# Kernel optimization log

Measured on AMD Instinct MI355X. Metric: run time of the kernel, lower is better.

## Reference

```python
import jax, jax.numpy as jnp
import numpy as np
from jax import lax

B, C, H, W = 16, 128, 96, 96
G, S = 4, 2            # DySample groups, scale
CO = 2 * G * S * S     # offset channels = 32
COUT = 64              # EUCB2 out_channels
BN_EPS = 1e-5


def conv2d(x, w, pad=0, dil=1, groups=1):
    return lax.conv_general_dilated(
        x, w, (1, 1), [(pad, pad), (pad, pad)],
        rhs_dilation=(dil, dil), feature_group_count=groups,
        dimension_numbers=('NCHW', 'OIHW', 'NCHW'))


def init_pos():
    # torch: arange((-s+1)/2,(s-1)/2+1)/s ; meshgrid ij ; stack ; transpose(1,2) ; repeat(1,G,1)
    h = (jnp.arange(S, dtype=jnp.float32) - (S - 1) / 2) / S
    gy, gx = jnp.meshgrid(h, h, indexing='ij')
    m = jnp.stack([gy, gx])                 # [2,S,S]
    m = jnp.swapaxes(m, 1, 2)               # transpose(1,2)
    m = jnp.tile(m, (1, G, 1))              # [2, S*G, S]
    return m.reshape(1, -1, 1, 1)           # [1, 2*G*S^2, 1, 1]


def grid_sample_border(x, grid):
    # x: [N,Cg,H,W], grid: [N,Ho,Wo,2] (x,y in [-1,1]), align_corners=False, border pad
    N, Cg, Hi, Wi = x.shape
    Ho, Wo = grid.shape[1], grid.shape[2]
    ix = jnp.clip(((grid[..., 0] + 1.0) * Wi - 1.0) * 0.5, 0.0, Wi - 1.0)
    iy = jnp.clip(((grid[..., 1] + 1.0) * Hi - 1.0) * 0.5, 0.0, Hi - 1.0)
    x0f = jnp.floor(ix); y0f = jnp.floor(iy)
    wx = (ix - x0f)[:, None]                # [N,1,Ho,Wo]
    wy = (iy - y0f)[:, None]
    x0 = jnp.clip(x0f.astype(jnp.int32), 0, Wi - 1)
    x1 = jnp.clip(x0 + 1, 0, Wi - 1)
    y0 = jnp.clip(y0f.astype(jnp.int32), 0, Hi - 1)
    y1 = jnp.clip(y0 + 1, 0, Hi - 1)
    flat = x.reshape(N, Cg, Hi * Wi)

    def gather(yi, xi):
        idx = (yi * Wi + xi).reshape(N, -1)
        return jax.vmap(lambda f, i: f[:, i])(flat, idx).reshape(N, Cg, Ho, Wo)

    v00 = gather(y0, x0); v01 = gather(y0, x1)
    v10 = gather(y1, x0); v11 = gather(y1, x1)
    return (v00 * (1 - wx) * (1 - wy) + v01 * wx * (1 - wy)
            + v10 * (1 - wx) * wy + v11 * wx * wy)


def setup_inputs() -> dict:
    key = jax.random.key(0)
    ks = jax.random.split(key, 11)
    inp = {
        'x': jax.random.normal(ks[0], (B, C, H, W), jnp.float32),
        'Wo1': jax.random.normal(ks[1], (CO, C, 1, 1), jnp.float32) * 0.001,
        'bo1': jnp.zeros((CO,), jnp.float32),
        'Wo2': jax.random.normal(ks[2], (CO, CO, 3, 3), jnp.float32) * 0.001,
        'Wdw': jax.random.normal(ks[3], (C, 1, 3, 3), jnp.float32) * 0.3,
        'bn_gamma': jax.random.uniform(ks[4], (C,), jnp.float32) * 0.5 + 0.75,
        'bn_beta': jax.random.normal(ks[5], (C,), jnp.float32) * 0.1,
        'bn_mean': jax.random.normal(ks[6], (C,), jnp.float32) * 0.1,
        'bn_var': jax.random.uniform(ks[7], (C,), jnp.float32) * 0.5 + 0.5,
        'Wpw': jax.random.normal(ks[8], (COUT, C, 1, 1), jnp.float32) / np.sqrt(C),
        'bpw': jax.random.normal(ks[9], (COUT,), jnp.float32) * 0.01,
    }
    return inp


def reference(x, Wo1, bo1, Wo2, Wdw, bn_gamma, bn_beta, bn_mean, bn_var, Wpw, bpw):
    # ---- offset branch: 1x1 conv (+bias) -> 3x3 dilated(2) conv (no bias) ----
    off = conv2d(x, Wo1) + bo1[:, None, None]
    off = conv2d(off, Wo2, pad=2, dil=2)
    offset = off / G + init_pos()                    # [B, 2*G*S^2, H, W]

    # ---- DySample.sample ----
    Bc, _, Hc, Wc = offset.shape
    offset = offset.reshape(Bc, 2, G * S * S, Hc, Wc)
    ar_h = jnp.arange(Hc, dtype=jnp.float32)
    ar_w = jnp.arange(Wc, dtype=jnp.float32)
    ch = ar_h + jnp.sin(jnp.pi * (ar_h + 1.0) / Hc)
    cw = ar_w + jnp.sin(jnp.pi * (ar_w + 1.0) / Wc)
    # channel 0 -> x coord (varies with w), channel 1 -> y coord (varies with h)
    base = jnp.stack([jnp.broadcast_to(cw[None, :], (Hc, Wc)),
                      jnp.broadcast_to(ch[:, None], (Hc, Wc))])   # [2,H,W]
    norm = jnp.array([Wc, Hc], jnp.float32).reshape(1, 2, 1, 1, 1)
    coords = 2.0 * (base[None, :, None] + offset) / norm - 1.0     # [B,2,G*S^2,H,W]

    # pixel_shuffle(scale=S) on [B, 2*G*S^2, H, W]
    coords = coords.reshape(Bc, 2, G, S, S, Hc, Wc)
    coords = coords.transpose(0, 1, 2, 5, 3, 6, 4)                 # [B,2,G,H,S,W,S]
    coords = coords.reshape(Bc, 2, G, S * Hc, S * Wc)
    grid = coords.transpose(0, 2, 3, 4, 1).reshape(Bc * G, S * Hc, S * Wc, 2)

    up = grid_sample_border(x.reshape(Bc * G, C // G, Hc, Wc), grid)
    up = up.reshape(Bc, C, S * Hc, S * Wc)                         # [B,C,2H,2W]

    # ---- EUCB2: depthwise conv -> BN -> ReLU -> channel_shuffle(C) -> 1x1 conv ----
    y = conv2d(up, Wdw, pad=1, groups=C)
    y = (y - bn_mean[:, None, None]) * (bn_gamma[:, None, None]
        * lax.rsqrt(bn_var + BN_EPS)[:, None, None]) + bn_beta[:, None, None]
    y = jax.nn.relu(y)
    # channel_shuffle with groups == num_channels => channels_per_group = 1 => identity
    out = conv2d(y, Wpw) + bpw[:, None, None]
    return out
```

## Files before the change

kernel.cpp:

```cpp
#include <hip/hip_runtime.h>
#include <math.h>

typedef _Float16 f16x8 __attribute__((ext_vector_type(8)));
typedef _Float16 f16x2 __attribute__((ext_vector_type(2)));
typedef float f32x4 __attribute__((ext_vector_type(4)));

namespace {
constexpr int B_ = 16, C_ = 128, H_ = 96, W_ = 96;
constexpr int HW_ = H_ * W_;
constexpr int G_ = 4, S_ = 2;
constexpr int CO_ = 32;
constexpr int COUT_ = 64;
constexpr int HO_ = 192, WO_ = 192;
constexpr int HWO_ = HO_ * WO_;
constexpr int CPG_ = C_ / G_;
constexpr int TH_ = 8, TW_ = 32;
constexpr int HALO_H = TH_ + 2, HALO_W = TW_ + 2;
constexpr int NPOS = HALO_H * HALO_W;
constexpr int NITEM = NPOS * 4;
constexpr int TILES = (WO_ / TW_) * (HO_ / TH_);
constexpr int BPI = HW_ / 256;
constexpr int XPB = HW_ / 64;

constexpr size_t WS_XT     = 0;
constexpr size_t WS_OFF1T  = 9437184;
constexpr size_t WS_COORDS = 11796480;
constexpr size_t WS_WPWH   = 16515072;
constexpr size_t WS_WO1H   = 16519168;
constexpr size_t WS_WO2H   = 16521216;
constexpr size_t WS_WDWSH  = 16525824;
constexpr size_t WS_BIAS2H = 16526400;
constexpr size_t WS_Y      = 16526464;
constexpr size_t Y_FULL_F  = (size_t)B_ * G_ * HWO_ * CPG_ / 2;
constexpr size_t NEED_FULL = (WS_Y + Y_FULL_F) * 4;
constexpr size_t NEED_MID  = (WS_Y + Y_FULL_F / 2) * 4;

constexpr int PREP_N = 8192 + 4096 + 9216 + 1152 + 128;
}

__device__ __forceinline__ f16x8 splat8(_Float16 s) {
  return (f16x8){s, s, s, s, s, s, s, s};
}

__global__ __launch_bounds__(256) void k_prep(
    const float* __restrict__ Wpw, const float* __restrict__ Wo1,
    const float* __restrict__ Wo2, const float* __restrict__ Wdw,
    const float* __restrict__ bn_gamma, const float* __restrict__ bn_beta,
    const float* __restrict__ bn_mean, const float* __restrict__ bn_var,
    _Float16* __restrict__ wpwH, _Float16* __restrict__ wo1H,
    _Float16* __restrict__ wo2H, _Float16* __restrict__ wdwSh,
    _Float16* __restrict__ bias2h) {
  int i = blockIdx.x * 256 + threadIdx.x;
  if (i < 8192) {
    wpwH[i] = (_Float16)Wpw[i];
  } else if (i < 8192 + 4096) {
    int j = i - 8192;
    wo1H[j] = (_Float16)Wo1[j];
  } else if (i < 8192 + 4096 + 9216) {
    int j = i - 8192 - 4096;
    int o = j / 288, r = j % 288;
    int tap = r / 32, ci = r % 32;
    wo2H[j] = (_Float16)Wo2[o * 288 + ci * 9 + tap];
  } else if (i < 8192 + 4096 + 9216 + 1152) {
    int j = i - 8192 - 4096 - 9216;
    int c = j / 9, t = j % 9;
    float sc = bn_gamma[c] * rsqrtf(bn_var[c] + 1e-5f);
    wdwSh[t * C_ + c] = (_Float16)(Wdw[j] * sc);
  } else if (i < PREP_N) {
    int c = i - (8192 + 4096 + 9216 + 1152);
    float sc = bn_gamma[c] * rsqrtf(bn_var[c] + 1e-5f);
    bias2h[c] = (_Float16)(bn_beta[c] - bn_mean[c] * sc);
  }
}

__global__ __launch_bounds__(256, 4) void k_xpose(const float* __restrict__ x,
                                                  _Float16* __restrict__ xT) {
  __shared__ float t[64][130];
  int bid = blockIdx.x;
  int swz = (bid & 7) * (B_ * XPB / 8) + (bid >> 3);
  int b = swz / XPB, px0 = (swz % XPB) * 64;
  int tid = threadIdx.x;
  int lane = tid & 63, wv = tid >> 6;
  const float* xb = x + (size_t)b * C_ * HW_ + px0 + lane;
  for (int c = wv; c < C_; c += 4) t[lane][c] = xb[(size_t)c * HW_];
  __syncthreads();
  _Float16* ob = xT + ((size_t)b * HW_ + px0) * C_;
#pragma unroll
  for (int k = 0; k < 4; ++k) {
    int cid = tid + 256 * k;
    int px = cid >> 4, part = cid & 15;
    f16x8 v;
#pragma unroll
    for (int j = 0; j < 8; ++j) v[j] = (_Float16)t[px][part * 8 + j];
    *(f16x8*)&ob[(size_t)px * C_ + part * 8] = v;
  }
}

__global__ __launch_bounds__(256, 4) void k_off1m(
    const _Float16* __restrict__ xT, const _Float16* __restrict__ wo1H,
    const float* __restrict__ bo1, _Float16* __restrict__ off1t) {
  __shared__ float clds[32][257];
  int bid = blockIdx.x;
  int swz = (bid & 7) * (B_ * BPI / 8) + (bid >> 3);
  int b = swz / BPI, p0 = (swz % BPI) * 256;
  int tid = threadIdx.x;
  int lane = tid & 63, wv_ = tid >> 6;
  int lr = lane & 15, lk = lane >> 4;

  f32x4 acc[4][2];
#pragma unroll
  for (int mt = 0; mt < 4; ++mt)
#pragma unroll
    for (int nt = 0; nt < 2; ++nt) acc[mt][nt] = (f32x4){0.f, 0.f, 0.f, 0.f};

  const _Float16* xb = xT + ((size_t)b * HW_ + p0) * C_;
#pragma unroll
  for (int kk = 0; kk < 4; ++kk) {
    f16x8 afr[4];
#pragma unroll
    for (int mt = 0; mt < 4; ++mt)
      afr[mt] = *(const f16x8*)&xb[(size_t)((wv_ * 4 + mt) * 16 + lr) * C_ +
                                   kk * 32 + lk * 8];
#pragma unroll
    for (int nt = 0; nt < 2; ++nt) {
      f16x8 bfr = *(const f16x8*)&wo1H[(nt * 16 + lr) * C_ + kk * 32 + lk * 8];
#pragma unroll
      for (int mt = 0; mt < 4; ++mt)
        acc[mt][nt] = __builtin_amdgcn_mfma_f32_16x16x32_f16(afr[mt], bfr,
                                                             acc[mt][nt], 0, 0, 0);
    }
  }
#pragma unroll
  for (int nt = 0; nt < 2; ++nt)
#pragma unroll
    for (int mt = 0; mt < 4; ++mt)
#pragma unroll
      for (int r = 0; r < 4; ++r)
        clds[nt * 16 + lr][(wv_ * 4 + mt) * 16 + lk * 4 + r] = acc[mt][nt][r];
  __syncthreads();
  _Float16* orow = off1t + ((size_t)b * HW_ + p0 + tid) * 32;
#pragma unroll
  for (int q = 0; q < 4; ++q) {
    f16x8 v;
#pragma unroll
    for (int j = 0; j < 8; ++j)
      v[j] = (_Float16)(clds[q * 8 + j][tid] + bo1[q * 8 + j]);
    *(f16x8*)&orow[q * 8] = v;
  }
}

__global__ __launch_bounds__(256, 4) void k_coordsm(
    const _Float16* __restrict__ off1t, const _Float16* __restrict__ wo2H,
    float* __restrict__ coords) {
  __shared__ float clds[32][257];
  int bid = blockIdx.x;
  int swz = (bid & 7) * (B_ * BPI / 8) + (bid >> 3);
  int b = swz / BPI, p0 = (swz % BPI) * 256;
  int tid = threadIdx.x;
  int lane = tid & 63, wv_ = tid >> 6;
  int lr = lane & 15, lk = lane >> 4;

  f32x4 acc[4][2];
#pragma unroll
  for (int mt = 0; mt < 4; ++mt)
#pragma unroll
    for (int nt = 0; nt < 2; ++nt) acc[mt][nt] = (f32x4){0.f, 0.f, 0.f, 0.f};

  const _Float16* ob = off1t + (size_t)b * HW_ * 32;
  int hh[4], ww[4];
#pragma unroll
  for (int mt = 0; mt < 4; ++mt) {
    int px = p0 + (wv_ * 4 + mt) * 16 + lr;
    hh[mt] = px / W_;
    ww[mt] = px % W_;
  }
#pragma unroll
  for (int tap = 0; tap < 9; ++tap) {
    int dy2 = (tap / 3 - 1) * 2, dx2 = (tap % 3 - 1) * 2;
    f16x8 afr[4];
#pragma unroll
    for (int mt = 0; mt < 4; ++mt) {
      int h2 = hh[mt] + dy2, w2 = ww[mt] + dx2;
      f16x8 a = {};
      if ((unsigned)h2 < (unsigned)H_ && (unsigned)w2 < (unsigned)W_)
        a = *(const f16x8*)&ob[(size_t)(h2 * W_ + w2) * 32 + lk * 8];
      afr[mt] = a;
    }
#pragma unroll
    for (int nt = 0; nt < 2; ++nt) {
      f16x8 bfr = *(const f16x8*)&wo2H[(nt * 16 + lr) * 288 + tap * 32 + lk * 8];
#pragma unroll
      for (int mt = 0; mt < 4; ++mt)
        acc[mt][nt] = __builtin_amdgcn_mfma_f32_16x16x32_f16(afr[mt], bfr,
                                                             acc[mt][nt], 0, 0, 0);
    }
  }
#pragma unroll
  for (int nt = 0; nt < 2; ++nt)
#pragma unroll
    for (int mt = 0; mt < 4; ++mt)
#pragma unroll
      for (int r = 0; r < 4; ++r)
        clds[nt * 16 + lr][(wv_ * 4 + mt) * 16 + lk * 4 + r] = acc[mt][nt][r];
  __syncthreads();

  int px = p0 + tid;
  int h = px / W_, w = px % W_;
  float cwv = (float)w + sinf((float)M_PI * (float)(w + 1) / (float)W_);
  float chv = (float)h + sinf((float)M_PI * (float)(h + 1) / (float)H_);
  float* cb = coords + (size_t)b * G_ * HWO_ * 2;
#pragma unroll
  for (int g = 0; g < G_; ++g) {
#pragma unroll
    for (int sh = 0; sh < S_; ++sh) {
#pragma unroll
      for (int sw = 0; sw < S_; ++sw) {
        int idx = g * 4 + sh * 2 + sw;
        float offx = clds[idx][tid] * 0.25f + (sw ? 0.25f : -0.25f);
        float offy = clds[16 + idx][tid] * 0.25f + (sh ? 0.25f : -0.25f);
        float ix = fminf(fmaxf(cwv + offx - 0.5f, 0.f), (float)(W_ - 1));
        float iy = fminf(fmaxf(chv + offy - 0.5f, 0.f), (float)(H_ - 1));
        float2* dst = (float2*)(cb + (((size_t)g * HO_ + 2 * h + sh) * WO_
                                      + 2 * w + sw) * 2);
        *dst = (float2){ix, iy};
      }
    }
  }
}

__global__ __launch_bounds__(256, 6) void k_sample(
    const _Float16* __restrict__ xT, const float* __restrict__ coords,
    const _Float16* __restrict__ wdwSh, const _Float16* __restrict__ bias2h,
    _Float16* __restrict__ y, int b0, int nimg) {
  __shared__ __align__(16) _Float16 up4[4 * NPOS * 8 + 832];

  int NWG = nimg * TILES;
  int bid = blockIdx.x;
  int swz = (bid & 7) * (NWG >> 3) + (bid >> 3);
  int bl = swz / TILES;
  int b = b0 + bl;
  int t = swz % TILES;
  int oh0 = (t / (WO_ / TW_)) * TH_;
  int ow0 = (t % (WO_ / TW_)) * TW_;
  int tid = threadIdx.x;
  int py = tid >> 5, px = tid & 31;
  int p_out = (oh0 + py) * WO_ + ow0 + px;

  const _Float16* xbase = xT + (size_t)b * HW_ * C_;
  for (int g = 0; g < G_; ++g) {
    __syncthreads();
    const float* cbase = coords + (((size_t)b * G_ + g) * HWO_) * 2;
    const _Float16* xg = xbase + g * CPG_;
#pragma unroll
    for (int r = 0; r < 6; ++r) {
      int wi = tid + r * 256;
      if (r == 5 && wi >= NITEM) continue;
      int p = wi >> 2, cq = wi & 3;
      int hy = oh0 + p / HALO_W - 1;
      int hx = ow0 + p % HALO_W - 1;
      f16x8 v = {};
      if (hy >= 0 && hy < HO_ && hx >= 0 && hx < WO_) {
        float2 c2 = *(const float2*)&cbase[((size_t)hy * WO_ + hx) * 2];
        float ix = c2.x, iy = c2.y;
        float x0f = floorf(ix), y0f = floorf(iy);
        float wx = ix - x0f, wy = iy - y0f;
        int x0 = (int)x0f, y0 = (int)y0f;
        int x1 = min(x0 + 1, W_ - 1);
        int y1 = min(y0 + 1, H_ - 1);
        f16x8 h00 = splat8((_Float16)((1.f - wx) * (1.f - wy)));
        f16x8 h01 = splat8((_Float16)(wx * (1.f - wy)));
        f16x8 h10 = splat8((_Float16)((1.f - wx) * wy));
        f16x8 h11 = splat8((_Float16)(wx * wy));
        const _Float16* xc = xg + cq * 8;
        f16x8 a00 = *(const f16x8*)&xc[(size_t)(y0 * W_ + x0) * C_];
        f16x8 a01 = *(const f16x8*)&xc[(size_t)(y0 * W_ + x1) * C_];
        f16x8 a10 = *(const f16x8*)&xc[(size_t)(y1 * W_ + x0) * C_];
        f16x8 a11 = *(const f16x8*)&xc[(size_t)(y1 * W_ + x1) * C_];
        v = a00 * h00 + a01 * h01 + a10 * h10 + a11 * h11;
      }
      *(f16x8*)&up4[((size_t)cq * NPOS + p) * 8] = v;
    }
    __syncthreads();

#pragma unroll
    for (int q = 0; q < 4; ++q) {
      f16x8 acc = *(const f16x8*)&bias2h[g * CPG_ + q * 8];
#pragma unroll
      for (int tt = 0; tt < 9; ++tt) {
        int dy = tt / 3, dx = tt % 3;
        f16x8 pk = *(const f16x8*)
            &up4[((size_t)q * NPOS + (py + dy) * HALO_W + px + dx) * 8];
        f16x8 wv = *(const f16x8*)&wdwSh[tt * C_ + g * CPG_ + q * 8];
        acc += pk * wv;
      }
      f16x8 yv;
#pragma unroll
      for (int j = 0; j < 8; ++j)
        yv[j] = acc[j] > (_Float16)0.f ? acc[j] : (_Float16)0.f;
      *(f16x8*)&y[(((size_t)(bl * G_ + g) * 4 + q) * HWO_ + p_out) * 8] = yv;
    }
  }
}

__global__ __launch_bounds__(256, 4) void k_gemm(
    const _Float16* __restrict__ y, const _Float16* __restrict__ wpwH,
    const float* __restrict__ bpw, float* __restrict__ out, int b0, int nimg) {
  __shared__ float clds16[16][257];

  int NWG = nimg * TILES;
  int bid = blockIdx.x;
  int swz = (bid & 7) * (NWG >> 3) + (bid >> 3);
  int bl = swz / TILES;
  int b = b0 + bl;
  int p0 = (swz % TILES) * 256;
  int tid = threadIdx.x;
  int lane = tid & 63, wv_ = tid >> 6;
  int lr = lane & 15, lk = lane >> 4;

  f32x4 acc[4][4];
#pragma unroll
  for (int mt = 0; mt < 4; ++mt)
#pragma unroll
    for (int nt = 0; nt < 4; ++nt) acc[mt][nt] = (f32x4){0.f, 0.f, 0.f, 0.f};

  const _Float16* ybl = y + (size_t)bl * G_ * 4 * HWO_ * 8;
#pragma unroll
  for (int kk = 0; kk < 4; ++kk) {
    f16x8 afr[4];
#pragma unroll
    for (int mt = 0; mt < 4; ++mt)
      afr[mt] = *(const f16x8*)&ybl[(((size_t)(kk * 4 + lk) * HWO_) + p0 +
                                     (wv_ * 4 + mt) * 16 + lr) * 8];
#pragma unroll
    for (int nt = 0; nt < 4; ++nt) {
      f16x8 bfr = *(const f16x8*)&wpwH[(nt * 16 + lr) * C_ + kk * CPG_ + lk * 8];
#pragma unroll
      for (int mt = 0; mt < 4; ++mt)
        acc[mt][nt] = __builtin_amdgcn_mfma_f32_16x16x32_f16(afr[mt], bfr,
                                                             acc[mt][nt], 0, 0, 0);
    }
  }
#pragma unroll
  for (int hq = 0; hq < 4; ++hq) {
    if (hq) __syncthreads();
#pragma unroll
    for (int mt = 0; mt < 4; ++mt) {
#pragma unroll
      for (int r = 0; r < 4; ++r)
        clds16[lr][(wv_ * 4 + mt) * 16 + lk * 4 + r] = acc[mt][hq][r];
    }
    __syncthreads();
#pragma unroll
    for (int i = 0; i < 16; ++i) {
      int o = hq * 16 + i;
      out[((size_t)b * COUT_ + o) * HWO_ + p0 + tid] = clds16[i][tid] + bpw[o];
    }
  }
}

extern "C" void kernel_launch(void* const* d_in, const int* in_sizes, int n_in,
                              void* d_out, int out_size, void* d_ws, size_t ws_size,
                              hipStream_t stream) {
  const float* x        = (const float*)d_in[0];
  const float* Wo1      = (const float*)d_in[1];
  const float* bo1      = (const float*)d_in[2];
  const float* Wo2      = (const float*)d_in[3];
  const float* Wdw      = (const float*)d_in[4];
  const float* bn_gamma = (const float*)d_in[5];
  const float* bn_beta  = (const float*)d_in[6];
  const float* bn_mean  = (const float*)d_in[7];
  const float* bn_var   = (const float*)d_in[8];
  const float* Wpw      = (const float*)d_in[9];
  const float* bpw      = (const float*)d_in[10];
  float* out = (float*)d_out;

  float* ws = (float*)d_ws;
  _Float16* xT     = (_Float16*)(ws + WS_XT);
  _Float16* off1t  = (_Float16*)(ws + WS_OFF1T);
  float* coords    = ws + WS_COORDS;
  _Float16* wpwH   = (_Float16*)(ws + WS_WPWH);
  _Float16* wo1H   = (_Float16*)(ws + WS_WO1H);
  _Float16* wo2H   = (_Float16*)(ws + WS_WO2H);
  _Float16* wdwSh  = (_Float16*)(ws + WS_WDWSH);
  _Float16* bias2h = (_Float16*)(ws + WS_BIAS2H);

  int chunk;
  _Float16* yb;
  if (ws_size >= NEED_FULL)      { chunk = 16; yb = (_Float16*)(ws + WS_Y); }
  else if (ws_size >= NEED_MID)  { chunk = 8;  yb = (_Float16*)(ws + WS_Y); }
  else                           { chunk = 1;  yb = (_Float16*)(ws + WS_OFF1T); }

  k_prep   <<<(PREP_N + 255) / 256, 256, 0, stream>>>(
      Wpw, Wo1, Wo2, Wdw, bn_gamma, bn_beta, bn_mean, bn_var,
      wpwH, wo1H, wo2H, wdwSh, bias2h);
  k_xpose  <<<B_ * XPB, 256, 0, stream>>>(x, xT);
  k_off1m  <<<B_ * BPI, 256, 0, stream>>>(xT, wo1H, bo1, off1t);
  k_coordsm<<<B_ * BPI, 256, 0, stream>>>(off1t, wo2H, coords);
  for (int c0 = 0; c0 < B_; c0 += chunk) {
    k_sample<<<chunk * TILES, 256, 0, stream>>>(xT, coords, wdwSh, bias2h, yb,
                                                c0, chunk);
    k_gemm  <<<chunk * TILES, 256, 0, stream>>>(yb, wpwH, bpw, out, c0, chunk);
  }
}
```

Before: 192.8 us.

## Merge sample and GEMM kernels into one launch with double-buffered image pipeline

```diff
diff --git a/kernel.cpp b/kernel.cpp
--- a/kernel.cpp
+++ b/kernel.cpp
@@ -31,9 +31,9 @@
 constexpr size_t WS_WDWSH  = 16525824;
 constexpr size_t WS_BIAS2H = 16526400;
 constexpr size_t WS_Y      = 16526464;
-constexpr size_t Y_FULL_F  = (size_t)B_ * G_ * HWO_ * CPG_ / 2;
-constexpr size_t NEED_FULL = (WS_Y + Y_FULL_F) * 4;
-constexpr size_t NEED_MID  = (WS_Y + Y_FULL_F / 2) * 4;
+constexpr size_t IMG_YF16  = (size_t)G_ * 4 * HWO_ * 8;
+constexpr int PIPE_P = 4;
+constexpr size_t NEED_PIPE = (WS_Y + 2 * PIPE_P * IMG_YF16 / 2) * 4;
 
 constexpr int PREP_N = 8192 + 4096 + 9216 + 1152 + 128;
 }
@@ -228,132 +228,132 @@
   }
 }
 
-__global__ __launch_bounds__(256, 6) void k_sample(
+__global__ __launch_bounds__(256, 6) void k_sg(
     const _Float16* __restrict__ xT, const float* __restrict__ coords,
     const _Float16* __restrict__ wdwSh, const _Float16* __restrict__ bias2h,
-    _Float16* __restrict__ y, int b0, int nimg) {
-  __shared__ __align__(16) _Float16 up4[4 * NPOS * 8 + 832];
-
-  int NWG = nimg * TILES;
+    const _Float16* __restrict__ wpwH, const float* __restrict__ bpw,
+    float* __restrict__ out, _Float16* __restrict__ ys,
+    const _Float16* __restrict__ yg, int sb0, int snimg, int gb0, int gnimg) {
+  __shared__ __align__(16) unsigned char pool[23424];
+  int nsb = snimg * TILES;
   int bid = blockIdx.x;
-  int swz = (bid & 7) * (NWG >> 3) + (bid >> 3);
-  int bl = swz / TILES;
-  int b = b0 + bl;
-  int t = swz % TILES;
-  int oh0 = (t / (WO_ / TW_)) * TH_;
-  int ow0 = (t % (WO_ / TW_)) * TW_;
-  int tid = threadIdx.x;
-  int py = tid >> 5, px = tid & 31;
-  int p_out = (oh0 + py) * WO_ + ow0 + px;
-
-  const _Float16* xbase = xT + (size_t)b * HW_ * C_;
-  for (int g = 0; g < G_; ++g) {
-    __syncthreads();
-    const float* cbase = coords + (((size_t)b * G_ + g) * HWO_) * 2;
-    const _Float16* xg = xbase + g * CPG_;
-#pragma unroll
-    for (int r = 0; r < 6; ++r) {
-      int wi = tid + r * 256;
-      if (r == 5 && wi >= NITEM) continue;
-      int p = wi >> 2, cq = wi & 3;
-      int hy = oh0 + p / HALO_W - 1;
-      int hx = ow0 + p % HALO_W - 1;
-      f16x8 v = {};
-      if (hy >= 0 && hy < HO_ && hx >= 0 && hx < WO_) {
-        float2 c2 = *(const float2*)&cbase[((size_t)hy * WO_ + hx) * 2];
-        float ix = c2.x, iy = c2.y;
-        float x0f = floorf(ix), y0f = floorf(iy);
-        float wx = ix - x0f, wy = iy - y0f;
-        int x0 = (int)x0f, y0 = (int)y0f;
-        int x1 = min(x0 + 1, W_ - 1);
-        int y1 = min(y0 + 1, H_ - 1);
-        f16x8 h00 = splat8((_Float16)((1.f - wx) * (1.f - wy)));
-        f16x8 h01 = splat8((_Float16)(wx * (1.f - wy)));
-        f16x8 h10 = splat8((_Float16)((1.f - wx) * wy));
-        f16x8 h11 = splat8((_Float16)(wx * wy));
-        const _Float16* xc = xg + cq * 8;
-        f16x8 a00 = *(const f16x8*)&xc[(size_t)(y0 * W_ + x0) * C_];
-        f16x8 a01 = *(const f16x8*)&xc[(size_t)(y0 * W_ + x1) * C_];
-        f16x8 a10 = *(const f16x8*)&xc[(size_t)(y1 * W_ + x0) * C_];
-        f16x8 a11 = *(const f16x8*)&xc[(size_t)(y1 * W_ + x1) * C_];
-        v = a00 * h00 + a01 * h01 + a10 * h10 + a11 * h11;
-      }
-      *(f16x8*)&up4[((size_t)cq * NPOS + p) * 8] = v;
-    }
-    __syncthreads();
-
-#pragma unroll
-    for (int q = 0; q < 4; ++q) {
-      f16x8 acc = *(const f16x8*)&bias2h[g * CPG_ + q * 8];
-#pragma unroll
-      for (int tt = 0; tt < 9; ++tt) {
-        int dy = tt / 3, dx = tt % 3;
-        f16x8 pk = *(const f16x8*)
-            &up4[((size_t)q * NPOS + (py + dy) * HALO_W + px + dx) * 8];
-        f16x8 wv = *(const f16x8*)&wdwSh[tt * C_ + g * CPG_ + q * 8];
-        acc += pk * wv;
-      }
-      f16x8 yv;
-#pragma unroll
-      for (int j = 0; j < 8; ++j)
-        yv[j] = acc[j] > (_Float16)0.f ? acc[j] : (_Float16)0.f;
-      *(f16x8*)&y[(((size_t)(bl * G_ + g) * 4 + q) * HWO_ + p_out) * 8] = yv;
-    }
-  }
-}
-
-__global__ __launch_bounds__(256, 4) void k_gemm(
-    const _Float16* __restrict__ y, const _Float16* __restrict__ wpwH,
-    const float* __restrict__ bpw, float* __restrict__ out, int b0, int nimg) {
-  __shared__ float clds16[16][257];
-
-  int NWG = nimg * TILES;
-  int bid = blockIdx.x;
-  int swz = (bid & 7) * (NWG >> 3) + (bid >> 3);
-  int bl = swz / TILES;
-  int b = b0 + bl;
-  int p0 = (swz % TILES) * 256;
   int tid = threadIdx.x;
   int lane = tid & 63, wv_ = tid >> 6;
   int lr = lane & 15, lk = lane >> 4;
 
-  f32x4 acc[4][4];
-#pragma unroll
-  for (int mt = 0; mt < 4; ++mt)
-#pragma unroll
-    for (int nt = 0; nt < 4; ++nt) acc[mt][nt] = (f32x4){0.f, 0.f, 0.f, 0.f};
-
-  const _Float16* ybl = y + (size_t)bl * G_ * 4 * HWO_ * 8;
-#pragma unroll
-  for (int kk = 0; kk < 4; ++kk) {
-    f16x8 afr[4];
+  if (bid < nsb) {
+    _Float16* up4 = (_Float16*)pool;
+    int swz = (bid & 7) * (nsb >> 3) + (bid >> 3);
+    int bl = swz / TILES;
+    int b = sb0 + bl;
+    int t = swz % TILES;
+    int oh0 = (t / (WO_ / TW_)) * TH_;
+    int ow0 = (t % (WO_ / TW_)) * TW_;
+    int py = tid >> 5, px = tid & 31;
+    int p_out = (oh0 + py) * WO_ + ow0 + px;
+
+    const _Float16* xbase = xT + (size_t)b * HW_ * C_;
+    _Float16* ydst = ys + (size_t)bl * IMG_YF16;
+    for (int g = 0; g < G_; ++g) {
+      __syncthreads();
+      const float* cbase = coords + (((size_t)b * G_ + g) * HWO_) * 2;
+      const _Float16* xg = xbase + g * CPG_;
+#pragma unroll
+      for (int r = 0; r < 6; ++r) {
+        int wi = tid + r * 256;
+        if (r == 5 && wi >= NITEM) continue;
+        int p = wi >> 2, cq = wi & 3;
+        int hy = oh0 + p / HALO_W - 1;
+        int hx = ow0 + p % HALO_W - 1;
+        f16x8 v = {};
+        if (hy >= 0 && hy < HO_ && hx >= 0 && hx < WO_) {
+          float2 c2 = *(const float2*)&cbase[((size_t)hy * WO_ + hx) * 2];
+          float ix = c2.x, iy = c2.y;
+          float x0f = floorf(ix), y0f = floorf(iy);
+          float wx = ix - x0f, wy = iy - y0f;
+          int x0 = (int)x0f, y0 = (int)y0f;
+          int x1 = min(x0 + 1, W_ - 1);
+          int y1 = min(y0 + 1, H_ - 1);
+          f16x8 h00 = splat8((_Float16)((1.f - wx) * (1.f - wy)));
+          f16x8 h01 = splat8((_Float16)(wx * (1.f - wy)));
+          f16x8 h10 = splat8((_Float16)((1.f - wx) * wy));
+          f16x8 h11 = splat8((_Float16)(wx * wy));
+          const _Float16* xc = xg + cq * 8;
+          f16x8 a00 = *(const f16x8*)&xc[(size_t)(y0 * W_ + x0) * C_];
+          f16x8 a01 = *(const f16x8*)&xc[(size_t)(y0 * W_ + x1) * C_];
+          f16x8 a10 = *(const f16x8*)&xc[(size_t)(y1 * W_ + x0) * C_];
+          f16x8 a11 = *(const f16x8*)&xc[(size_t)(y1 * W_ + x1) * C_];
+          v = a00 * h00 + a01 * h01 + a10 * h10 + a11 * h11;
+        }
+        *(f16x8*)&up4[((size_t)cq * NPOS + p) * 8] = v;
+      }
+      __syncthreads();
+
+#pragma unroll
+      for (int q = 0; q < 4; ++q) {
+        f16x8 acc = *(const f16x8*)&bias2h[g * CPG_ + q * 8];
+#pragma unroll
+        for (int tt = 0; tt < 9; ++tt) {
+          int dy = tt / 3, dx = tt % 3;
+          f16x8 pk = *(const f16x8*)
+              &up4[((size_t)q * NPOS + (py + dy) * HALO_W + px + dx) * 8];
+          f16x8 wv = *(const f16x8*)&wdwSh[tt * C_ + g * CPG_ + q * 8];
+          acc += pk * wv;
+        }
+        f16x8 yv;
+#pragma unroll
+        for (int j = 0; j < 8; ++j)
+          yv[j] = acc[j] > (_Float16)0.f ? acc[j] : (_Float16)0.f;
+        *(f16x8*)&ydst[(((size_t)g * 4 + q) * HWO_ + p_out) * 8] = yv;
+      }
+    }
+  } else {
+    float (*clds16)[257] = (float(*)[257])pool;
+    int gbid = bid - nsb;
+    int ngb = gnimg * TILES;
+    int swz = (gbid & 7) * (ngb >> 3) + (gbid >> 3);
+    int bl = swz / TILES;
+    int b = gb0 + bl;
+    int p0 = (swz % TILES) * 256;
+
+    f32x4 acc[4][4];
 #pragma unroll
     for (int mt = 0; mt < 4; ++mt)
-      afr[mt] = *(const f16x8*)&ybl[(((size_t)(kk * 4 + lk) * HWO_) + p0 +
-                                     (wv_ * 4 + mt) * 16 + lr) * 8];
-#pragma unroll
-    for (int nt = 0; nt < 4; ++nt) {
-      f16x8 bfr = *(const f16x8*)&wpwH[(nt * 16 + lr) * C_ + kk * CPG_ + lk * 8];
+#pragma unroll
+      for (int nt = 0; nt < 4; ++nt) acc[mt][nt] = (f32x4){0.f, 0.f, 0.f, 0.f};
+
+    const _Float16* ybl = yg + (size_t)bl * IMG_YF16;
+#pragma unroll
+    for (int kk = 0; kk < 4; ++kk) {
+      f16x8 afr[4];
 #pragma unroll
       for (int mt = 0; mt < 4; ++mt)
-        acc[mt][nt] = __builtin_amdgcn_mfma_f32_16x16x32_f16(afr[mt], bfr,
-                                                             acc[mt][nt], 0, 0, 0);
-    }
-  }
-#pragma unroll
-  for (int hq = 0; hq < 4; ++hq) {
-    if (hq) __syncthreads();
-#pragma unroll
-    for (int mt = 0; mt < 4; ++mt) {
-#pragma unroll
-      for (int r = 0; r < 4; ++r)
-        clds16[lr][(wv_ * 4 + mt) * 16 + lk * 4 + r] = acc[mt][hq][r];
-    }
-    __syncthreads();
-#pragma unroll
-    for (int i = 0; i < 16; ++i) {
-      int o = hq * 16 + i;
-      out[((size_t)b * COUT_ + o) * HWO_ + p0 + tid] = clds16[i][tid] + bpw[o];
+        afr[mt] = *(const f16x8*)&ybl[(((size_t)(kk * 4 + lk) * HWO_) + p0 +
+                                       (wv_ * 4 + mt) * 16 + lr) * 8];
+#pragma unroll
+      for (int nt = 0; nt < 4; ++nt) {
+        f16x8 bfr = *(const f16x8*)&wpwH[(nt * 16 + lr) * C_ + kk * CPG_ + lk * 8];
+#pragma unroll
+        for (int mt = 0; mt < 4; ++mt)
+          acc[mt][nt] = __builtin_amdgcn_mfma_f32_16x16x32_f16(afr[mt], bfr,
+                                                               acc[mt][nt], 0, 0, 0);
+      }
+    }
+#pragma unroll
+    for (int hq = 0; hq < 4; ++hq) {
+      if (hq) __syncthreads();
+#pragma unroll
+      for (int mt = 0; mt < 4; ++mt) {
+#pragma unroll
+        for (int r = 0; r < 4; ++r)
+          clds16[lr][(wv_ * 4 + mt) * 16 + lk * 4 + r] = acc[mt][hq][r];
+      }
+      __syncthreads();
+#pragma unroll
+      for (int i = 0; i < 16; ++i) {
+        int o = hq * 16 + i;
+        out[((size_t)b * COUT_ + o) * HWO_ + p0 + tid] = clds16[i][tid] + bpw[o];
+      }
     }
   }
 }
@@ -384,21 +384,34 @@
   _Float16* wdwSh  = (_Float16*)(ws + WS_WDWSH);
   _Float16* bias2h = (_Float16*)(ws + WS_BIAS2H);
 
-  int chunk;
-  _Float16* yb;
-  if (ws_size >= NEED_FULL)      { chunk = 16; yb = (_Float16*)(ws + WS_Y); }
-  else if (ws_size >= NEED_MID)  { chunk = 8;  yb = (_Float16*)(ws + WS_Y); }
-  else                           { chunk = 1;  yb = (_Float16*)(ws + WS_OFF1T); }
-
   k_prep   <<<(PREP_N + 255) / 256, 256, 0, stream>>>(
       Wpw, Wo1, Wo2, Wdw, bn_gamma, bn_beta, bn_mean, bn_var,
       wpwH, wo1H, wo2H, wdwSh, bias2h);
   k_xpose  <<<B_ * XPB, 256, 0, stream>>>(x, xT);
   k_off1m  <<<B_ * BPI, 256, 0, stream>>>(xT, wo1H, bo1, off1t);
   k_coordsm<<<B_ * BPI, 256, 0, stream>>>(off1t, wo2H, coords);
-  for (int c0 = 0; c0 < B_; c0 += chunk) {
-    k_sample<<<chunk * TILES, 256, 0, stream>>>(xT, coords, wdwSh, bias2h, yb,
-                                                c0, chunk);
-    k_gemm  <<<chunk * TILES, 256, 0, stream>>>(yb, wpwH, bpw, out, c0, chunk);
-  }
-}
+
+  if (ws_size >= NEED_PIPE) {
+    constexpr int P = PIPE_P;
+    _Float16* y0 = (_Float16*)(ws + WS_Y);
+    _Float16* y1 = y0 + (size_t)P * IMG_YF16;
+    k_sg<<<P * TILES, 256, 0, stream>>>(xT, coords, wdwSh, bias2h, wpwH, bpw,
+                                        out, y0, y0, 0, P, 0, 0);
+    k_sg<<<2 * P * TILES, 256, 0, stream>>>(xT, coords, wdwSh, bias2h, wpwH,
+                                            bpw, out, y1, y0, P, P, 0, P);
+    k_sg<<<2 * P * TILES, 256, 0, stream>>>(xT, coords, wdwSh, bias2h, wpwH,
+                                            bpw, out, y0, y1, 2 * P, P, P, P);
+    k_sg<<<2 * P * TILES, 256, 0, stream>>>(xT, coords, wdwSh, bias2h, wpwH,
+                                            bpw, out, y1, y0, 3 * P, P, 2 * P, P);
+    k_sg<<<P * TILES, 256, 0, stream>>>(xT, coords, wdwSh, bias2h, wpwH, bpw,
+                                        out, y1, y1, 0, 0, 3 * P, P);
+  } else {
+    _Float16* ya = (_Float16*)(ws + WS_OFF1T);
+    for (int i = 0; i < B_; ++i) {
+      k_sg<<<TILES, 256, 0, stream>>>(xT, coords, wdwSh, bias2h, wpwH, bpw,
+                                      out, ya, ya, i, 1, 0, 0);
+      k_sg<<<TILES, 256, 0, stream>>>(xT, coords, wdwSh, bias2h, wpwH, bpw,
+                                      out, ya, ya, 0, 0, i, 1);
+    }
+  }
+}
```

Result: slower. 315.9 us (+63.8%).
